# Optimization experiments

Hardware: AMD Instinct MI355X
Metric: run time of the kernel (lower is better)

## Reference

```python
import jax, jax.numpy as jnp
import numpy as np

B, S, T = 2048, 32, 32
D, H = 128, 256       # cle_dim, rnn_dim
VS, VT = 256, 256     # source/target char vocab
BOW = 1               # MorphoDataset.Factor.BOW


def setup_inputs() -> dict:
    key = jax.random.key(0)
    ks = jax.random.split(key, 16)
    n = lambda k, sh: (jax.random.normal(k, sh, jnp.float32) * 0.05)
    inp = {
        "src_emb": n(ks[0], (VS, D)),
        "tgt_emb": n(ks[1], (VT, D)),
        "enc_f_W": n(ks[2], (D, 3 * H)),
        "enc_f_U": n(ks[3], (H, 3 * H)),
        "enc_f_b": jnp.zeros((2, 3 * H), jnp.float32),
        "enc_b_W": n(ks[4], (D, 3 * H)),
        "enc_b_U": n(ks[5], (H, 3 * H)),
        "enc_b_b": jnp.zeros((2, 3 * H), jnp.float32),
        "dec_W": n(ks[6], (D + H, 3 * H)),
        "dec_U": n(ks[7], (H, 3 * H)),
        "dec_b": jnp.zeros((2, 3 * H), jnp.float32),
        "out_W": n(ks[8], (H, VT)),
        "out_b": jnp.zeros((VT,), jnp.float32),
        "att_src_W": n(ks[9], (H, H)),
        "att_src_b": jnp.zeros((H,), jnp.float32),
        "att_st_W": n(ks[10], (H, H)),
        "att_st_b": jnp.zeros((H,), jnp.float32),
        "att_v": n(ks[11], (H, 1)),
        "att_v_b": jnp.zeros((1,), jnp.float32),
        "source_ids": jax.random.randint(ks[12], (B, S), 0, VS, jnp.int32),
        "target_ids": jax.random.randint(ks[13], (B, T), 0, VT, jnp.int32),
    }
    return inp


def _gru_step(h, x, W, U, b):
    # Keras GRU, reset_after=True: separate input/recurrent biases b[0], b[1]
    gx = x @ W + b[0]
    gh = h @ U + b[1]
    xz, xr, xh = jnp.split(gx, 3, axis=-1)
    hz, hr, hh = jnp.split(gh, 3, axis=-1)
    z = jax.nn.sigmoid(xz + hz)
    r = jax.nn.sigmoid(xr + hr)
    c = jnp.tanh(xh + r * hh)
    return z * h + (1.0 - z) * c


def _gru_scan(x_tbd, W, U, b):
    # x_tbd: [S, B, D] -> outputs [S, B, H]
    h0 = jnp.zeros((x_tbd.shape[1], U.shape[0]), x_tbd.dtype)
    def step(h, x):
        h = _gru_step(h, x, W, U, b)
        return h, h
    _, ys = jax.lax.scan(step, h0, x_tbd)
    return ys


def reference(src_emb, tgt_emb, enc_f_W, enc_f_U, enc_f_b, enc_b_W, enc_b_U, enc_b_b,
              dec_W, dec_U, dec_b, out_W, out_b, att_src_W, att_src_b,
              att_st_W, att_st_b, att_v, att_v_b, source_ids, target_ids):
    # ---- Encoder: bidirectional GRU, merge_mode='sum' ----
    x = src_emb[source_ids]                      # [B, S, D]
    x_t = jnp.transpose(x, (1, 0, 2))            # [S, B, D]
    fwd = _gru_scan(x_t, enc_f_W, enc_f_U, enc_f_b)
    bwd = _gru_scan(x_t[::-1], enc_b_W, enc_b_U, enc_b_b)[::-1]
    source_states = jnp.transpose(fwd + bwd, (1, 0, 2))  # [B, S, H]

    # projected source states are constant across decoder steps -> precompute
    proj_src = source_states @ att_src_W + att_src_b     # [B, S, H]

    def attend(inp, h):
        p = h @ att_st_W + att_st_b                      # [B, H]
        e = jnp.tanh(proj_src + p[:, None, :]) @ att_v + att_v_b  # [B, S, 1]
        w = jax.nn.softmax(e, axis=1)                    # softmax over source positions
        ctx = jnp.sum(source_states * w, axis=1)         # [B, H]
        return jnp.concatenate([inp, ctx], axis=1)       # [B, D+H]

    # ---- Decoder (teacher forcing) ----
    h0 = source_states[:, 0]                             # [B, H]
    bow = jnp.broadcast_to(tgt_emb[BOW], (source_ids.shape[0], tgt_emb.shape[1]))
    inp0 = attend(bow, h0)

    def dstep(carry, tgt_t):
        h, inp = carry
        h = _gru_step(h, inp, dec_W, dec_U, dec_b)       # GRUCell step
        logits = h @ out_W + out_b                       # [B, VT]
        nxt = attend(tgt_emb[tgt_t], h)
        return (h, nxt), logits

    _, logits = jax.lax.scan(dstep, (h0, inp0), jnp.transpose(target_ids))
    return jnp.transpose(logits, (1, 0, 2))              # [B, T, VT]
```

## Files before the change

### kernel.cpp

```cpp
#include <hip/hip_runtime.h>
#include <math.h>

#define B_  2048
#define S_  32
#define T_  32
#define D_  128
#define H_  256
#define G3  768
#define VT_ 256
#define BOW_ 1

typedef __attribute__((ext_vector_type(8))) short short8;
typedef __attribute__((ext_vector_type(4))) float f32x4;
typedef __attribute__((ext_vector_type(8))) unsigned short us8;
typedef unsigned short u16;

__device__ inline u16 f2bf(float x) {
  union { float f; unsigned u; } v; v.f = x;
  unsigned r = v.u + 0x7FFFu + ((v.u >> 16) & 1u);
  return (u16)(r >> 16);
}
__device__ inline float bf2f(u16 b) {
  union { unsigned u; float f; } v; v.u = ((unsigned)b) << 16; return v.f;
}
__device__ inline int swz(int r) { return ((r ^ (r >> 3)) & 7) << 3; }
__device__ inline float sigm(float x) { return 1.f / (1.f + expf(-x)); }

struct TMat { const float* src; u16* dhi; u16* dlo; int R; int C; int tile0; };
struct TPack { TMat m[10]; };

__global__ __launch_bounds__(256)
void wsplit_t(TPack P) {
  int bx = blockIdx.x;
  TMat M = P.m[0];
  #pragma unroll
  for (int i = 1; i < 10; i++) if (bx >= P.m[i].tile0) M = P.m[i];
  int ti = bx - M.tile0;
  int tilesR = M.R >> 6;
  int rt = ti % tilesR, ct = ti / tilesR;
  int r0 = rt * 64, c0 = ct * 64;
  __shared__ float ts[64][65];
  int tid = threadIdx.x;
  int cx = tid & 63, ry = tid >> 6;
  #pragma unroll
  for (int i = 0; i < 16; i++) {
    int r = ry * 16 + i;
    ts[r][cx] = M.src[(size_t)(r0 + r) * M.C + c0 + cx];
  }
  __syncthreads();
  int rx = tid & 63, cy = tid >> 6;
  #pragma unroll
  for (int i = 0; i < 16; i++) {
    int cc = cy * 16 + i;
    float v = ts[rx][cc];
    u16 hi = f2bf(v);
    size_t o = (size_t)(c0 + cc) * M.R + r0 + rx;
    M.dhi[o] = hi;
    M.dlo[o] = f2bf(v - bf2f(hi));
  }
}

__global__ __launch_bounds__(256)
void esplit(const float* a, const float* b, u16* ah, u16* al, u16* bh, u16* bl, int n) {
  int i = blockIdx.x * 256 + threadIdx.x;
  if (i >= 2 * n) return;
  const float* s = (i < n) ? a : b;
  u16* dh = (i < n) ? ah : bh;
  u16* dl = (i < n) ? al : bl;
  int j = (i < n) ? i : i - n;
  float v = s[j];
  u16 hi = f2bf(v);
  dh[j] = hi; dl[j] = f2bf(v - bf2f(hi));
}

struct PLeg {
  const u16* Ahi; const u16* Alo; int lda;
  const u16* Bthi; const u16* Btlo; int ldb;
  const float* bias; void* C; int ldc; int cmode;
  int M, N, K;
};

__global__ __launch_bounds__(256)
void gemm_pl(PLeg l0, PLeg l1) {
  PLeg L = blockIdx.z ? l1 : l0;
  int n0 = blockIdx.x * 128; if (n0 >= L.N) return;
  int m0 = blockIdx.y * 128; if (m0 >= L.M) return;
  __shared__ u16 As[128 * 64];
  __shared__ u16 Bs[128 * 64];
  int tid = threadIdx.x;
  int lane = tid & 63, wv = tid >> 6;
  int wr = (wv >> 1) * 64, wc = (wv & 1) * 64;
  int fr = lane & 15, fk = (lane >> 4) * 8;
  f32x4 acc[4][4];
  #pragma unroll
  for (int m = 0; m < 4; m++)
    #pragma unroll
    for (int n = 0; n < 4; n++) acc[m][n] = (f32x4){0.f, 0.f, 0.f, 0.f};

  int s_row = tid >> 1, s_part = tid & 1;

  for (int k0 = 0; k0 < L.K; k0 += 32) {
    if (k0) __syncthreads();
    int swA = swz(s_row);
    {
      const u16* src = (s_part ? L.Alo : L.Ahi) + (size_t)(m0 + s_row) * L.lda + k0;
      #pragma unroll
      for (int q = 0; q < 4; q++)
        *(us8*)&As[(s_row * 64 + s_part * 32 + q * 8) ^ swA] = *(const us8*)(src + q * 8);
    }
    {
      const u16* src = (s_part ? L.Btlo : L.Bthi) + (size_t)(n0 + s_row) * L.ldb + k0;
      #pragma unroll
      for (int q = 0; q < 4; q++)
        *(us8*)&Bs[(s_row * 64 + s_part * 32 + q * 8) ^ swA] = *(const us8*)(src + q * 8);
    }
    __syncthreads();
    short8 bhi[4], blo[4];
    #pragma unroll
    for (int n = 0; n < 4; n++) {
      int cc = wc + n * 16 + fr; int sw = swz(cc);
      bhi[n] = *(const short8*)&Bs[(cc * 64 + fk) ^ sw];
      blo[n] = *(const short8*)&Bs[(cc * 64 + 32 + fk) ^ sw];
    }
    #pragma unroll
    for (int m = 0; m < 4; m++) {
      int r = wr + m * 16 + fr; int sw = swz(r);
      short8 ahi = *(const short8*)&As[(r * 64 + fk) ^ sw];
      short8 alo = *(const short8*)&As[(r * 64 + 32 + fk) ^ sw];
      #pragma unroll
      for (int n = 0; n < 4; n++) {
        acc[m][n] = __builtin_amdgcn_mfma_f32_16x16x32_bf16(ahi, bhi[n], acc[m][n], 0, 0, 0);
        acc[m][n] = __builtin_amdgcn_mfma_f32_16x16x32_bf16(ahi, blo[n], acc[m][n], 0, 0, 0);
        acc[m][n] = __builtin_amdgcn_mfma_f32_16x16x32_bf16(alo, bhi[n], acc[m][n], 0, 0, 0);
      }
    }
  }
  int rbase = (lane >> 4) * 4;
  #pragma unroll
  for (int m = 0; m < 4; m++)
    #pragma unroll
    for (int rr = 0; rr < 4; rr++) {
      int row = m0 + wr + m * 16 + rbase + rr;
      #pragma unroll
      for (int n = 0; n < 4; n++) {
        int col = n0 + wc + n * 16 + fr;
        float v = acc[m][n][rr];
        if (L.bias) v += L.bias[col];
        if (L.cmode == 0)      ((float*)L.C)[(size_t)row * L.ldc + col] = v;
        else if (L.cmode == 1) ((u16*)L.C)[(size_t)row * L.ldc + col] = f2bf(v);
        else {
          size_t o = (((size_t)(row & (B_ - 1))) * T_ + (row >> 11)) * VT_ + col;
          ((float*)L.C)[o] = v;
        }
      }
    }
}

struct GruDesc {
  const u16 *a0H, *a0L;
  const u16 *a1H, *a1L;
  const u16 *b0H, *b0L;
  const u16 *b1H, *b1L;
  const float *gxT;
  const float *bias0, *bias1;
  const float *hold;
  const u16 *holdH, *holdL;
  float *hnew;
  u16 *hh, *hl;
  u16 *ssH, *ssL;
  const int *ids;
  int ssmode;
  int sidx, rev;
};

template<int MODE>
__global__ __launch_bounds__(256)
void gru_step(GruDesc d0, GruDesc d1) {
  GruDesc D = blockIdx.z ? d1 : d0;
  constexpr int KT  = MODE ? 512 : 256;
  constexpr int KT8 = KT / 8;
  constexpr int MF  = MODE ? 1 : 2;
  constexpr int NST = KT / 32;
  __shared__ __align__(16) u16 As[2 * 32 * KT];

  int m0 = blockIdx.y * 32;
  int tid = threadIdx.x;
  int lane = tid & 63, wv = tid >> 6;
  int fr = lane & 15, kq = lane >> 4;
  int jn, rb0;
  if (MODE == 0) { jn = blockIdx.x * 64 + wv * 16 + fr; rb0 = 0; }
  else           { jn = blockIdx.x * 32 + (wv & 1) * 16 + fr; rb0 = (wv >> 1) * 16; }

  constexpr int PER_T = (2 * 32 * KT8) / 256;
  #pragma unroll
  for (int i = 0; i < PER_T; i++) {
    int s = tid + i * 256;
    int p = s / (32 * KT8);
    int rem = s - p * (32 * KT8);
    int row = rem / KT8;
    int kb = rem - row * KT8;
    int k = kb * 8;
    const u16* src;
    if (MODE == 0) {
      src = (p ? D.a0L : D.a0H) + (size_t)(m0 + row) * 256 + k;
    } else {
      src = (k < 256) ? (p ? D.a0L : D.a0H) + (size_t)(m0 + row) * 256 + k
                      : (p ? D.a1L : D.a1H) + (size_t)(m0 + row) * 256 + (k - 256);
    }
    *(us8*)&As[(s ^ (row & 7)) * 8] = *(const us8*)src;
  }
  __syncthreads();

  f32x4 acc[4][MF];
  #pragma unroll
  for (int a = 0; a < 4; a++)
    #pragma unroll
    for (int mf = 0; mf < MF; mf++) acc[a][mf] = (f32x4){0.f, 0.f, 0.f, 0.f};

  #pragma unroll
  for (int i = 0; i < NST; i++) {
    const u16 *BH, *BL; int bk, ai2;
    if (MODE == 0)    { BH = D.b0H; BL = D.b0L; bk = i * 32; ai2 = 2; }
    else if (i < 8)   { BH = D.b0H; BL = D.b0L; bk = i * 32; ai2 = 2; }
    else              { BH = D.b1H; BL = D.b1L; bk = (i - 8) * 32; ai2 = 3; }
    short8 ah[MF], al[MF];
    #pragma unroll
    for (int mf = 0; mf < MF; mf++) {
      int rp = rb0 + mf * 16 + fr;
      int kb = i * 4 + kq;
      ah[mf] = *(const short8*)&As[((rp * KT8 + kb) ^ (fr & 7)) * 8];
      al[mf] = *(const short8*)&As[((32 * KT8 + rp * KT8 + kb) ^ (fr & 7)) * 8];
    }
    #pragma unroll
    for (int st = 0; st < 3; st++) {
      size_t ro = (size_t)(st * 256 + jn) * 256 + bk + kq * 8;
      short8 bh = *(const short8*)(BH + ro);
      short8 bl = *(const short8*)(BL + ro);
      int ai = (st < 2) ? st : ai2;
      #pragma unroll
      for (int mf = 0; mf < MF; mf++) {
        acc[ai][mf] = __builtin_amdgcn_mfma_f32_16x16x32_bf16(ah[mf], bh, acc[ai][mf], 0, 0, 0);
        acc[ai][mf] = __builtin_amdgcn_mfma_f32_16x16x32_bf16(ah[mf], bl, acc[ai][mf], 0, 0, 0);
        acc[ai][mf] = __builtin_amdgcn_mfma_f32_16x16x32_bf16(al[mf], bh, acc[ai][mf], 0, 0, 0);
      }
    }
  }

  int rbase = kq * 4;
  int j = jn;
  float b0z = D.bias0[j],       b1z = D.bias1[j];
  float b0r = D.bias0[256 + j], b1r = D.bias1[256 + j];
  float b0c = D.bias0[512 + j], b1c = D.bias1[512 + j];
  #pragma unroll
  for (int mf = 0; mf < MF; mf++)
    #pragma unroll
    for (int rr = 0; rr < 4; rr++) {
      int b = m0 + rb0 + mf * 16 + rbase + rr;
      size_t o = (size_t)b * H_ + j;
      int id;
      if (MODE == 0) id = D.ids[b * S_ + (D.rev ? (S_ - 1 - D.sidx) : D.sidx)];
      else           id = (D.sidx == 0) ? BOW_ : D.ids[b * T_ + D.sidx - 1];
      const float* T = D.gxT + (size_t)id * G3;
      float z = sigm(acc[0][mf][rr] + T[j] + b0z + b1z);
      float r = sigm(acc[1][mf][rr] + T[256 + j] + b0r + b1r);
      float xc = T[512 + j] + b0c + (MODE ? acc[3][mf][rr] : 0.f);
      float c = tanhf(xc + r * (acc[2][mf][rr] + b1c));
      float hprev = D.hold ? D.hold[o] : (bf2f(D.holdH[o]) + bf2f(D.holdL[o]));
      float hn = z * hprev + (1.f - z) * c;
      D.hnew[o] = hn;
      u16 hi = f2bf(hn);
      D.hh[o] = hi; D.hl[o] = f2bf(hn - bf2f(hi));
      if (MODE == 0) {
        if (D.ssmode == 1) {
          D.ssH[o] = hi; D.ssL[o] = f2bf(hn - bf2f(hi));
        } else if (D.ssmode == 2) {
          float v = bf2f(D.ssH[o]) + bf2f(D.ssL[o]) + hn;
          u16 vh = f2bf(v);
          D.ssH[o] = vh; D.ssL[o] = f2bf(v - bf2f(vh));
        }
      }
    }
}

__global__ __launch_bounds__(256)
void attend_k(const u16* __restrict__ projbf, const u16* __restrict__ ssH,
              const float* __restrict__ p, const float* __restrict__ att_v,
              u16* __restrict__ ctxh, u16* __restrict__ ctxl) {
  int b = blockIdx.x;
  int tid = threadIdx.x;
  int lane = tid & 63;
  int wv = tid >> 6;
  __shared__ float e_s[S_];
  __shared__ float w_s[S_];
  float pq[4], vq[4];
  #pragma unroll
  for (int q = 0; q < 4; q++) {
    pq[q] = p[(size_t)b * H_ + q * 64 + lane];
    vq[q] = att_v[q * 64 + lane];
  }
  float pv[8][4];
  #pragma unroll
  for (int i = 0; i < 8; i++) {
    const u16* pr = projbf + ((size_t)(wv * 8 + i) * B_ + b) * H_;
    #pragma unroll
    for (int q = 0; q < 4; q++) pv[i][q] = bf2f(pr[q * 64 + lane]);
  }
  u16 sv[S_];
  #pragma unroll
  for (int s = 0; s < S_; s++) sv[s] = ssH[((size_t)s * B_ + b) * H_ + tid];

  #pragma unroll
  for (int i = 0; i < 8; i++) {
    float part = 0.f;
    #pragma unroll
    for (int q = 0; q < 4; q++)
      part += tanhf(pv[i][q] + pq[q]) * vq[q];
    #pragma unroll
    for (int off = 32; off; off >>= 1)
      part += __shfl_xor(part, off);
    if (lane == 0) e_s[wv * 8 + i] = part;
  }
  __syncthreads();
  float m = -1e30f;
  #pragma unroll
  for (int s = 0; s < S_; s++) m = fmaxf(m, e_s[s]);
  float den = 0.f;
  #pragma unroll
  for (int s = 0; s < S_; s++) den += expf(e_s[s] - m);
  if (tid < S_) w_s[tid] = expf(e_s[tid] - m) / den;
  __syncthreads();
  float acc = 0.f;
  #pragma unroll
  for (int s = 0; s < S_; s++)
    acc = fmaf(w_s[s], bf2f(sv[s]), acc);
  u16 hi = f2bf(acc);
  size_t o = (size_t)b * H_ + tid;
  ctxh[o] = hi; ctxl[o] = f2bf(acc - bf2f(hi));
}

extern "C" void kernel_launch(void* const* d_in, const int* in_sizes, int n_in,
                              void* d_out, int out_size, void* d_ws, size_t ws_size,
                              hipStream_t stream) {
  const float* src_emb   = (const float*)d_in[0];
  const float* tgt_emb   = (const float*)d_in[1];
  const float* enc_f_W   = (const float*)d_in[2];
  const float* enc_f_U   = (const float*)d_in[3];
  const float* enc_f_b   = (const float*)d_in[4];
  const float* enc_b_W   = (const float*)d_in[5];
  const float* enc_b_U   = (const float*)d_in[6];
  const float* enc_b_b   = (const float*)d_in[7];
  const float* dec_W     = (const float*)d_in[8];
  const float* dec_U     = (const float*)d_in[9];
  const float* dec_b     = (const float*)d_in[10];
  const float* out_W     = (const float*)d_in[11];
  const float* out_b     = (const float*)d_in[12];
  const float* att_src_W = (const float*)d_in[13];
  const float* att_src_b = (const float*)d_in[14];
  const float* att_st_W  = (const float*)d_in[15];
  const float* att_st_b  = (const float*)d_in[16];
  const float* att_v     = (const float*)d_in[17];
  const int* source_ids  = (const int*)d_in[19];
  const int* target_ids  = (const int*)d_in[20];
  float* out = (float*)d_out;

  char* base = (char*)d_ws;
  size_t off = 0;
  auto allocB = [&](size_t bytes) { void* p = base + off; off = (off + bytes + 255) & ~255UL; return p; };
  const size_t BH = (size_t)B_ * H_;

  u16* ssH    = (u16*)allocB((size_t)S_ * BH * 2);
  u16* ssL    = (u16*)allocB((size_t)S_ * BH * 2);
  u16* projbf = (u16*)allocB((size_t)S_ * BH * 2);
  float* pbuf = (float*)allocB(BH * 4);
  u16* ctxh = (u16*)allocB(BH * 2);
  u16* ctxl = (u16*)allocB(BH * 2);

  float* encF0 = (float*)allocB(2 * BH * 4);
  u16*  encPl0 = (u16*)allocB(4 * BH * 2);
  float* encF1 = (float*)allocB(2 * BH * 4);
  u16*  encPl1 = (u16*)allocB(4 * BH * 2);
  float* encF[2][2]  = { { encF0, encF0 + BH }, { encF1, encF1 + BH } };
  u16*  encH[2][2]   = { { encPl0, encPl0 + 2 * BH }, { encPl1, encPl1 + 2 * BH } };
  u16*  encL[2][2]   = { { encPl0 + BH, encPl0 + 3 * BH }, { encPl1 + BH, encPl1 + 3 * BH } };

  float* hDecF[2] = { (float*)allocB(BH * 4), (float*)allocB(BH * 4) };
  u16* hAllH = (u16*)allocB((size_t)T_ * BH * 2);
  u16* hAllL = (u16*)allocB((size_t)T_ * BH * 2);

  auto planes2 = [&](size_t n, u16*& h, u16*& l) { h = (u16*)allocB(n * 2); l = (u16*)allocB(n * 2); };
  u16 *UtFh,*UtFl,*UtBh,*UtBl,*WtFh,*WtFl,*WtBh,*WtBl;
  u16 *dUth,*dUtl,*dWcth,*dWctl,*dWxth,*dWxtl;
  u16 *oWth,*oWtl,*aStth,*aSttl,*aSrth,*aSrtl;
  u16 *sEh,*sEl,*tEh,*tEl;
  planes2((size_t)G3*H_, UtFh, UtFl);   planes2((size_t)G3*H_, UtBh, UtBl);
  planes2((size_t)G3*D_, WtFh, WtFl);   planes2((size_t)G3*D_, WtBh, WtBl);
  planes2((size_t)G3*H_, dUth, dUtl);   planes2((size_t)G3*H_, dWcth, dWctl);
  planes2((size_t)G3*D_, dWxth, dWxtl);
  planes2((size_t)H_*VT_, oWth, oWtl);
  planes2((size_t)H_*H_, aSrth, aSrtl);
  planes2((size_t)H_*H_, aStth, aSttl);
  planes2((size_t)VT_*D_, sEh, sEl);    planes2((size_t)VT_*D_, tEh, tEl);
  float* Tf = (float*)allocB((size_t)VT_ * G3 * 4);
  float* Tb = (float*)allocB((size_t)VT_ * G3 * 4);
  float* Td = (float*)allocB((size_t)VT_ * G3 * 4);

  TPack P;
  P.m[0] = { enc_f_U,          UtFh, UtFl, 256, 768, 0   };
  P.m[1] = { enc_b_U,          UtBh, UtBl, 256, 768, 48  };
  P.m[2] = { dec_U,            dUth, dUtl, 256, 768, 96  };
  P.m[3] = { dec_W + 128 * G3, dWcth, dWctl, 256, 768, 144 };
  P.m[4] = { enc_f_W,          WtFh, WtFl, 128, 768, 192 };
  P.m[5] = { enc_b_W,          WtBh, WtBl, 128, 768, 216 };
  P.m[6] = { dec_W,            dWxth, dWxtl, 128, 768, 240 };
  P.m[7] = { out_W,            oWth, oWtl, 256, 256, 264 };
  P.m[8] = { att_src_W,        aSrth, aSrtl, 256, 256, 280 };
  P.m[9] = { att_st_W,         aStth, aSttl, 256, 256, 296 };
  wsplit_t<<<312, 256, 0, stream>>>(P);
  esplit<<<(2 * VT_ * D_ + 255) / 256, 256, 0, stream>>>(src_emb, tgt_emb, sEh, sEl, tEh, tEl, VT_ * D_);

  {
    PLeg tf = { sEh, sEl, D_, WtFh, WtFl, D_, nullptr, Tf, G3, 0, VT_, G3, D_ };
    PLeg tb = { sEh, sEl, D_, WtBh, WtBl, D_, nullptr, Tb, G3, 0, VT_, G3, D_ };
    gemm_pl<<<dim3(6, 2, 2), 256, 0, stream>>>(tf, tb);
    PLeg td = { tEh, tEl, D_, dWxth, dWxtl, D_, nullptr, Td, G3, 0, VT_, G3, D_ };
    gemm_pl<<<dim3(6, 2, 1), 256, 0, stream>>>(td, td);
  }

  hipMemsetAsync(encF0, 0, 2 * BH * 4, stream);
  hipMemsetAsync(encPl0, 0, 4 * BH * 2, stream);

  for (int s = 0; s < S_; s++) {
    int p = s & 1;
    GruDesc dd[2];
    for (int d = 0; d < 2; d++) {
      GruDesc& D = dd[d];
      D.a0H = encH[p][d]; D.a0L = encL[p][d];
      D.a1H = nullptr; D.a1L = nullptr;
      D.b0H = d ? UtBh : UtFh; D.b0L = d ? UtBl : UtFl;
      D.b1H = nullptr; D.b1L = nullptr;
      D.gxT = d ? Tb : Tf;
      D.bias0 = d ? enc_b_b : enc_f_b;
      D.bias1 = (d ? enc_b_b : enc_f_b) + G3;
      D.hold = encF[p][d]; D.holdH = nullptr; D.holdL = nullptr;
      D.hnew = encF[p ^ 1][d];
      D.hh = encH[p ^ 1][d]; D.hl = encL[p ^ 1][d];
      int pos = d ? (S_ - 1 - s) : s;
      D.ssH = ssH + (size_t)pos * BH; D.ssL = ssL + (size_t)pos * BH;
      D.ids = source_ids;
      D.ssmode = (s < S_ / 2) ? 1 : 2;
      D.sidx = s; D.rev = d;
    }
    gru_step<0><<<dim3(4, 64, 2), 256, 0, stream>>>(dd[0], dd[1]);
  }

  {
    PLeg proj = { ssH, ssL, H_, aSrth, aSrtl, H_, att_src_b, projbf, H_, 1, S_ * B_, H_, H_ };
    PLeg p0   = { ssH, ssL, H_, aStth, aSttl, H_, att_st_b,  pbuf,   H_, 0, B_,      H_, H_ };
    gemm_pl<<<dim3(2, 512, 2), 256, 0, stream>>>(proj, p0);
  }
  attend_k<<<B_, 256, 0, stream>>>(projbf, ssH, pbuf, att_v, ctxh, ctxl);

  for (int t = 0; t < T_; t++) {
    int p = t & 1;
    GruDesc D = {};
    D.a0H = t ? hAllH + (size_t)(t - 1) * BH : ssH;
    D.a0L = t ? hAllL + (size_t)(t - 1) * BH : ssL;
    D.a1H = ctxh; D.a1L = ctxl;
    D.b0H = dUth;  D.b0L = dUtl;
    D.b1H = dWcth; D.b1L = dWctl;
    D.gxT = Td;
    D.bias0 = dec_b; D.bias1 = dec_b + G3;
    if (t == 0) { D.hold = nullptr; D.holdH = ssH; D.holdL = ssL; }
    else        { D.hold = hDecF[p]; D.holdH = nullptr; D.holdL = nullptr; }
    D.hnew = hDecF[p ^ 1];
    D.hh = hAllH + (size_t)t * BH; D.hl = hAllL + (size_t)t * BH;
    D.ssH = nullptr; D.ssL = nullptr;
    D.ids = target_ids;
    D.ssmode = 0; D.sidx = t; D.rev = 0;
    gru_step<1><<<dim3(8, 64, 1), 256, 0, stream>>>(D, D);

    if (t < T_ - 1) {
      PLeg LP = { hAllH + (size_t)t * BH, hAllL + (size_t)t * BH, H_,
                  aStth, aSttl, H_, att_st_b, pbuf, H_, 0, B_, H_, H_ };
      gemm_pl<<<dim3(2, 16, 1), 256, 0, stream>>>(LP, LP);
      attend_k<<<B_, 256, 0, stream>>>(projbf, ssH, pbuf, att_v, ctxh, ctxl);
    }
  }

  {
    PLeg LO = { hAllH, hAllL, H_, oWth, oWtl, H_, out_b, out, 0, 2, T_ * B_, VT_, H_ };
    gemm_pl<<<dim3(2, 512, 1), 256, 0, stream>>>(LO, LO);
  }
}
```

Before: 3.604 ms.

## Replace per-step GRU launches with persistent encoder and decoder kernels

```diff
diff --git a/kernel.cpp b/kernel.cpp
--- a/kernel.cpp
+++ b/kernel.cpp
@@ -15,6 +15,8 @@
 typedef __attribute__((ext_vector_type(8))) unsigned short us8;
 typedef unsigned short u16;
 
+#define MFMA16 __builtin_amdgcn_mfma_f32_16x16x32_bf16
+
 __device__ inline u16 f2bf(float x) {
   union { float f; unsigned u; } v; v.f = x;
   unsigned r = v.u + 0x7FFFu + ((v.u >> 16) & 1u);
@@ -24,6 +26,9 @@
   union { unsigned u; float f; } v; v.u = ((unsigned)b) << 16; return v.f;
 }
 __device__ inline int swz(int r) { return ((r ^ (r >> 3)) & 7) << 3; }
+__device__ inline int psl(int row, int j) {
+  return row * 256 + ((((j >> 3) ^ (row & 7)) << 3) | (j & 7));
+}
 __device__ inline float sigm(float x) { return 1.f / (1.f + expf(-x)); }
 
 struct TMat { const float* src; u16* dhi; u16* dlo; int R; int C; int tile0; };
@@ -129,9 +134,9 @@
       short8 alo = *(const short8*)&As[(r * 64 + 32 + fk) ^ sw];
       #pragma unroll
       for (int n = 0; n < 4; n++) {
-        acc[m][n] = __builtin_amdgcn_mfma_f32_16x16x32_bf16(ahi, bhi[n], acc[m][n], 0, 0, 0);
-        acc[m][n] = __builtin_amdgcn_mfma_f32_16x16x32_bf16(ahi, blo[n], acc[m][n], 0, 0, 0);
-        acc[m][n] = __builtin_amdgcn_mfma_f32_16x16x32_bf16(alo, bhi[n], acc[m][n], 0, 0, 0);
+        acc[m][n] = MFMA16(ahi, bhi[n], acc[m][n], 0, 0, 0);
+        acc[m][n] = MFMA16(ahi, blo[n], acc[m][n], 0, 0, 0);
+        acc[m][n] = MFMA16(alo, bhi[n], acc[m][n], 0, 0, 0);
       }
     }
   }
@@ -156,186 +161,332 @@
     }
 }
 
-struct GruDesc {
-  const u16 *a0H, *a0L;
-  const u16 *a1H, *a1L;
-  const u16 *b0H, *b0L;
-  const u16 *b1H, *b1L;
-  const float *gxT;
+struct EncMP {
+  const u16 *UH0, *UL0, *UH1, *UL1;
+  const float *gxT0, *gxT1;
   const float *bias0, *bias1;
-  const float *hold;
-  const u16 *holdH, *holdL;
-  float *hnew;
-  u16 *hh, *hl;
   u16 *ssH, *ssL;
   const int *ids;
-  int ssmode;
-  int sidx, rev;
 };
 
-template<int MODE>
-__global__ __launch_bounds__(256)
-void gru_step(GruDesc d0, GruDesc d1) {
-  GruDesc D = blockIdx.z ? d1 : d0;
-  constexpr int KT  = MODE ? 512 : 256;
-  constexpr int KT8 = KT / 8;
-  constexpr int MF  = MODE ? 1 : 2;
-  constexpr int NST = KT / 32;
-  __shared__ __align__(16) u16 As[2 * 32 * KT];
-
-  int m0 = blockIdx.y * 32;
-  int tid = threadIdx.x;
-  int lane = tid & 63, wv = tid >> 6;
-  int fr = lane & 15, kq = lane >> 4;
-  int jn, rb0;
-  if (MODE == 0) { jn = blockIdx.x * 64 + wv * 16 + fr; rb0 = 0; }
-  else           { jn = blockIdx.x * 32 + (wv & 1) * 16 + fr; rb0 = (wv >> 1) * 16; }
-
-  constexpr int PER_T = (2 * 32 * KT8) / 256;
-  #pragma unroll
-  for (int i = 0; i < PER_T; i++) {
-    int s = tid + i * 256;
-    int p = s / (32 * KT8);
-    int rem = s - p * (32 * KT8);
-    int row = rem / KT8;
-    int kb = rem - row * KT8;
-    int k = kb * 8;
-    const u16* src;
-    if (MODE == 0) {
-      src = (p ? D.a0L : D.a0H) + (size_t)(m0 + row) * 256 + k;
-    } else {
-      src = (k < 256) ? (p ? D.a0L : D.a0H) + (size_t)(m0 + row) * 256 + k
-                      : (p ? D.a1L : D.a1H) + (size_t)(m0 + row) * 256 + (k - 256);
-    }
-    *(us8*)&As[(s ^ (row & 7)) * 8] = *(const us8*)src;
-  }
+__global__ __launch_bounds__(256, 1)
+void enc_mono(EncMP P) {
+  __shared__ __align__(16) u16 hPl[2][2][4096];
+  __shared__ float hF[2][2048];
+  __shared__ int ids_l[256];
+  const int tid = threadIdx.x;
+  const int lane = tid & 63, wv = tid >> 6;
+  const int fr = lane & 15, kq = lane >> 4;
+  const int jb = wv * 64;
+  const int r0 = blockIdx.x * 8;
+
+  {
+    us8 z8 = {0,0,0,0,0,0,0,0};
+    us8* pb = (us8*)&hPl[0][0][0];
+    #pragma unroll
+    for (int i = 0; i < 8; i++) pb[i * 256 + tid] = z8;
+    f32x4 zf = {0.f,0.f,0.f,0.f};
+    f32x4* fb = (f32x4*)&hF[0][0];
+    #pragma unroll
+    for (int i = 0; i < 4; i++) fb[i * 256 + tid] = zf;
+  }
+  ids_l[tid] = P.ids[(r0 + (tid >> 5)) * S_ + (tid & 31)];
   __syncthreads();
 
-  f32x4 acc[4][MF];
-  #pragma unroll
-  for (int a = 0; a < 4; a++)
-    #pragma unroll
-    for (int mf = 0; mf < MF; mf++) acc[a][mf] = (f32x4){0.f, 0.f, 0.f, 0.f};
-
-  #pragma unroll
-  for (int i = 0; i < NST; i++) {
-    const u16 *BH, *BL; int bk, ai2;
-    if (MODE == 0)    { BH = D.b0H; BL = D.b0L; bk = i * 32; ai2 = 2; }
-    else if (i < 8)   { BH = D.b0H; BL = D.b0L; bk = i * 32; ai2 = 2; }
-    else              { BH = D.b1H; BL = D.b1L; bk = (i - 8) * 32; ai2 = 3; }
-    short8 ah[MF], al[MF];
-    #pragma unroll
-    for (int mf = 0; mf < MF; mf++) {
-      int rp = rb0 + mf * 16 + fr;
-      int kb = i * 4 + kq;
-      ah[mf] = *(const short8*)&As[((rp * KT8 + kb) ^ (fr & 7)) * 8];
-      al[mf] = *(const short8*)&As[((32 * KT8 + rp * KT8 + kb) ^ (fr & 7)) * 8];
-    }
-    #pragma unroll
-    for (int st = 0; st < 3; st++) {
-      size_t ro = (size_t)(st * 256 + jn) * 256 + bk + kq * 8;
-      short8 bh = *(const short8*)(BH + ro);
-      short8 bl = *(const short8*)(BL + ro);
-      int ai = (st < 2) ? st : ai2;
-      #pragma unroll
-      for (int mf = 0; mf < MF; mf++) {
-        acc[ai][mf] = __builtin_amdgcn_mfma_f32_16x16x32_bf16(ah[mf], bh, acc[ai][mf], 0, 0, 0);
-        acc[ai][mf] = __builtin_amdgcn_mfma_f32_16x16x32_bf16(ah[mf], bl, acc[ai][mf], 0, 0, 0);
-        acc[ai][mf] = __builtin_amdgcn_mfma_f32_16x16x32_bf16(al[mf], bh, acc[ai][mf], 0, 0, 0);
-      }
-    }
-  }
-
-  int rbase = kq * 4;
-  int j = jn;
-  float b0z = D.bias0[j],       b1z = D.bias1[j];
-  float b0r = D.bias0[256 + j], b1r = D.bias1[256 + j];
-  float b0c = D.bias0[512 + j], b1c = D.bias1[512 + j];
-  #pragma unroll
-  for (int mf = 0; mf < MF; mf++)
-    #pragma unroll
-    for (int rr = 0; rr < 4; rr++) {
-      int b = m0 + rb0 + mf * 16 + rbase + rr;
-      size_t o = (size_t)b * H_ + j;
-      int id;
-      if (MODE == 0) id = D.ids[b * S_ + (D.rev ? (S_ - 1 - D.sidx) : D.sidx)];
-      else           id = (D.sidx == 0) ? BOW_ : D.ids[b * T_ + D.sidx - 1];
-      const float* T = D.gxT + (size_t)id * G3;
-      float z = sigm(acc[0][mf][rr] + T[j] + b0z + b1z);
-      float r = sigm(acc[1][mf][rr] + T[256 + j] + b0r + b1r);
-      float xc = T[512 + j] + b0c + (MODE ? acc[3][mf][rr] : 0.f);
-      float c = tanhf(xc + r * (acc[2][mf][rr] + b1c));
-      float hprev = D.hold ? D.hold[o] : (bf2f(D.holdH[o]) + bf2f(D.holdL[o]));
-      float hn = z * hprev + (1.f - z) * c;
-      D.hnew[o] = hn;
-      u16 hi = f2bf(hn);
-      D.hh[o] = hi; D.hl[o] = f2bf(hn - bf2f(hi));
-      if (MODE == 0) {
-        if (D.ssmode == 1) {
-          D.ssH[o] = hi; D.ssL[o] = f2bf(hn - bf2f(hi));
-        } else if (D.ssmode == 2) {
-          float v = bf2f(D.ssH[o]) + bf2f(D.ssL[o]) + hn;
-          u16 vh = f2bf(v);
-          D.ssH[o] = vh; D.ssL[o] = f2bf(v - bf2f(vh));
+  float bz[2][4], br[2][4], bxc[2][4], bhc[2][4];
+  #pragma unroll
+  for (int d = 0; d < 2; d++) {
+    const float* b0 = d ? P.bias1 : P.bias0;
+    const float* b1 = b0 + G3;
+    #pragma unroll
+    for (int nt = 0; nt < 4; nt++) {
+      int j = jb + nt * 16 + fr;
+      bz[d][nt]  = b0[j] + b1[j];
+      br[d][nt]  = b0[256 + j] + b1[256 + j];
+      bxc[d][nt] = b0[512 + j];
+      bhc[d][nt] = b1[512 + j];
+    }
+  }
+
+  for (int s = 0; s < S_; s++) {
+    #pragma unroll 1
+    for (int d = 0; d < 2; d++) {
+      const u16* UH = d ? P.UH1 : P.UH0;
+      const u16* UL = d ? P.UL1 : P.UL0;
+      const float* gxT = d ? P.gxT1 : P.gxT0;
+      u16* hp0 = hPl[d][0];
+      u16* hp1 = hPl[d][1];
+      f32x4 acc[3][4];
+      #pragma unroll
+      for (int a = 0; a < 3; a++)
+        #pragma unroll
+        for (int nt = 0; nt < 4; nt++) acc[a][nt] = (f32x4){0.f,0.f,0.f,0.f};
+
+      #pragma unroll
+      for (int i = 0; i < 8; i++) {
+        int slot = (((i * 4 + kq) ^ (fr & 7)) << 3);
+        short8 ah = *(const short8*)&hp0[fr * 256 + slot];
+        short8 al = *(const short8*)&hp1[fr * 256 + slot];
+        #pragma unroll
+        for (int st = 0; st < 3; st++)
+          #pragma unroll
+          for (int nt = 0; nt < 4; nt++) {
+            size_t ro = (size_t)(st * 256 + jb + nt * 16 + fr) * 256 + i * 32 + kq * 8;
+            short8 bh = *(const short8*)(UH + ro);
+            short8 bl = *(const short8*)(UL + ro);
+            acc[st][nt] = MFMA16(ah, bh, acc[st][nt], 0, 0, 0);
+            acc[st][nt] = MFMA16(ah, bl, acc[st][nt], 0, 0, 0);
+            acc[st][nt] = MFMA16(al, bh, acc[st][nt], 0, 0, 0);
+          }
+      }
+      __syncthreads();
+      if (kq < 2) {
+        #pragma unroll
+        for (int rr = 0; rr < 4; rr++) {
+          int row = kq * 4 + rr;
+          int gb = r0 + row;
+          int id = ids_l[row * 32 + (d ? (31 - s) : s)];
+          const float* T = gxT + (size_t)id * G3;
+          int pos = d ? (31 - s) : s;
+          #pragma unroll
+          for (int nt = 0; nt < 4; nt++) {
+            int j = jb + nt * 16 + fr;
+            float z = sigm(acc[0][nt][rr] + T[j] + bz[d][nt]);
+            float r = sigm(acc[1][nt][rr] + T[256 + j] + br[d][nt]);
+            float c = tanhf(T[512 + j] + bxc[d][nt] + r * (acc[2][nt][rr] + bhc[d][nt]));
+            float hp = hF[d][row * 256 + j];
+            float hn = z * hp + (1.f - z) * c;
+            hF[d][row * 256 + j] = hn;
+            u16 hi = f2bf(hn);
+            u16 lo = f2bf(hn - bf2f(hi));
+            int ps = psl(row, j);
+            hp0[ps] = hi; hp1[ps] = lo;
+            size_t o = ((size_t)pos * B_ + gb) * 256 + j;
+            if (s < 16) {
+              P.ssH[o] = hi; P.ssL[o] = lo;
+            } else {
+              float v = bf2f(P.ssH[o]) + bf2f(P.ssL[o]) + hn;
+              u16 vh = f2bf(v);
+              P.ssH[o] = vh; P.ssL[o] = f2bf(v - bf2f(vh));
+            }
+          }
         }
       }
-    }
-}
-
-__global__ __launch_bounds__(256)
-void attend_k(const u16* __restrict__ projbf, const u16* __restrict__ ssH,
-              const float* __restrict__ p, const float* __restrict__ att_v,
-              u16* __restrict__ ctxh, u16* __restrict__ ctxl) {
-  int b = blockIdx.x;
-  int tid = threadIdx.x;
-  int lane = tid & 63;
-  int wv = tid >> 6;
-  __shared__ float e_s[S_];
-  __shared__ float w_s[S_];
-  float pq[4], vq[4];
-  #pragma unroll
-  for (int q = 0; q < 4; q++) {
-    pq[q] = p[(size_t)b * H_ + q * 64 + lane];
-    vq[q] = att_v[q * 64 + lane];
-  }
-  float pv[8][4];
-  #pragma unroll
-  for (int i = 0; i < 8; i++) {
-    const u16* pr = projbf + ((size_t)(wv * 8 + i) * B_ + b) * H_;
-    #pragma unroll
-    for (int q = 0; q < 4; q++) pv[i][q] = bf2f(pr[q * 64 + lane]);
-  }
-  u16 sv[S_];
-  #pragma unroll
-  for (int s = 0; s < S_; s++) sv[s] = ssH[((size_t)s * B_ + b) * H_ + tid];
-
-  #pragma unroll
-  for (int i = 0; i < 8; i++) {
-    float part = 0.f;
-    #pragma unroll
-    for (int q = 0; q < 4; q++)
-      part += tanhf(pv[i][q] + pq[q]) * vq[q];
-    #pragma unroll
-    for (int off = 32; off; off >>= 1)
-      part += __shfl_xor(part, off);
-    if (lane == 0) e_s[wv * 8 + i] = part;
-  }
+      __syncthreads();
+    }
+  }
+}
+
+struct DecMP {
+  const u16 *UH, *UL, *CH, *CL;
+  const float *gxT;
+  const float *bias;
+  const u16 *sWH, *sWL;
+  const float *stb;
+  const u16 *ssH, *ssL;
+  const u16 *projbf;
+  const float *attv;
+  u16 *hAH, *hAL;
+  const int *ids;
+};
+
+__global__ __launch_bounds__(256, 1)
+void dec_mono(DecMP P) {
+  __shared__ __align__(16) u16 hPl[2][4096];
+  __shared__ __align__(16) u16 cPl[2][4096];
+  __shared__ float hF[2048];
+  __shared__ float pS[2048];
+  __shared__ int ids_l[256];
+  const int tid = threadIdx.x;
+  const int lane = tid & 63, wv = tid >> 6;
+  const int fr = lane & 15, kq = lane >> 4;
+  const int jb = wv * 64;
+  const int r0 = blockIdx.x * 8;
+
+  {
+    us8 z8 = {0,0,0,0,0,0,0,0};
+    us8* pb = (us8*)&hPl[0][0];
+    #pragma unroll
+    for (int i = 0; i < 4; i++) pb[i * 256 + tid] = z8;
+    us8* cb = (us8*)&cPl[0][0];
+    #pragma unroll
+    for (int i = 0; i < 4; i++) cb[i * 256 + tid] = z8;
+  }
+  ids_l[tid] = P.ids[(r0 + (tid >> 5)) * T_ + (tid & 31)];
   __syncthreads();
-  float m = -1e30f;
-  #pragma unroll
-  for (int s = 0; s < S_; s++) m = fmaxf(m, e_s[s]);
-  float den = 0.f;
-  #pragma unroll
-  for (int s = 0; s < S_; s++) den += expf(e_s[s] - m);
-  if (tid < S_) w_s[tid] = expf(e_s[tid] - m) / den;
+  {
+    int row = tid >> 5;
+    int k = (tid & 31) * 8;
+    size_t go = ((size_t)(r0 + row)) * 256 + k;
+    us8 hv = *(const us8*)(P.ssH + go);
+    us8 lv = *(const us8*)(P.ssL + go);
+    int sl = row * 256 + ((((k >> 3) ^ (row & 7))) << 3);
+    *(us8*)&hPl[0][sl] = hv;
+    *(us8*)&hPl[1][sl] = lv;
+    #pragma unroll
+    for (int e = 0; e < 8; e++) hF[row * 256 + k + e] = bf2f(hv[e]) + bf2f(lv[e]);
+  }
+
+  float bz[4], br_[4], bxc[4], bhc[4], stbv[4];
+  #pragma unroll
+  for (int nt = 0; nt < 4; nt++) {
+    int j = jb + nt * 16 + fr;
+    bz[nt]  = P.bias[j] + P.bias[G3 + j];
+    br_[nt] = P.bias[256 + j] + P.bias[G3 + 256 + j];
+    bxc[nt] = P.bias[512 + j];
+    bhc[nt] = P.bias[G3 + 512 + j];
+    stbv[nt] = P.stb[j];
+  }
+  float vq[4];
+  #pragma unroll
+  for (int q = 0; q < 4; q++) vq[q] = P.attv[q * 64 + lane];
   __syncthreads();
-  float acc = 0.f;
-  #pragma unroll
-  for (int s = 0; s < S_; s++)
-    acc = fmaf(w_s[s], bf2f(sv[s]), acc);
-  u16 hi = f2bf(acc);
-  size_t o = (size_t)b * H_ + tid;
-  ctxh[o] = hi; ctxl[o] = f2bf(acc - bf2f(hi));
+
+  auto lp_attend = [&]() {
+    f32x4 pa[4];
+    #pragma unroll
+    for (int nt = 0; nt < 4; nt++) pa[nt] = (f32x4){0.f,0.f,0.f,0.f};
+    #pragma unroll
+    for (int i = 0; i < 8; i++) {
+      int slot = (((i * 4 + kq) ^ (fr & 7)) << 3);
+      short8 ah = *(const short8*)&hPl[0][fr * 256 + slot];
+      short8 al = *(const short8*)&hPl[1][fr * 256 + slot];
+      #pragma unroll
+      for (int nt = 0; nt < 4; nt++) {
+        size_t ro = (size_t)(jb + nt * 16 + fr) * 256 + i * 32 + kq * 8;
+        short8 bh = *(const short8*)(P.sWH + ro);
+        short8 bl = *(const short8*)(P.sWL + ro);
+        pa[nt] = MFMA16(ah, bh, pa[nt], 0, 0, 0);
+        pa[nt] = MFMA16(ah, bl, pa[nt], 0, 0, 0);
+        pa[nt] = MFMA16(al, bh, pa[nt], 0, 0, 0);
+      }
+    }
+    if (kq < 2) {
+      #pragma unroll
+      for (int rr = 0; rr < 4; rr++) {
+        int row = kq * 4 + rr;
+        #pragma unroll
+        for (int nt = 0; nt < 4; nt++) {
+          int j = jb + nt * 16 + fr;
+          pS[row * 256 + j] = pa[nt][rr] + stbv[nt];
+        }
+      }
+    }
+    __syncthreads();
+    #pragma unroll 1
+    for (int u = 0; u < 2; u++) {
+      int row = wv * 2 + u;
+      int gb = r0 + row;
+      float pq[4];
+      #pragma unroll
+      for (int q = 0; q < 4; q++) pq[q] = pS[row * 256 + q * 64 + lane];
+      float sc[S_];
+      #pragma unroll
+      for (int s2 = 0; s2 < S_; s2++) {
+        const u16* pr = P.projbf + ((size_t)s2 * B_ + gb) * 256;
+        float part = 0.f;
+        #pragma unroll
+        for (int q = 0; q < 4; q++)
+          part += tanhf(bf2f(pr[q * 64 + lane]) + pq[q]) * vq[q];
+        #pragma unroll
+        for (int off = 32; off; off >>= 1)
+          part += __shfl_xor(part, off);
+        sc[s2] = part;
+      }
+      float m = -1e30f;
+      #pragma unroll
+      for (int s2 = 0; s2 < S_; s2++) m = fmaxf(m, sc[s2]);
+      float den = 0.f;
+      #pragma unroll
+      for (int s2 = 0; s2 < S_; s2++) { sc[s2] = expf(sc[s2] - m); den += sc[s2]; }
+      float inv = 1.f / den;
+      float cacc[4] = {0.f, 0.f, 0.f, 0.f};
+      #pragma unroll
+      for (int s2 = 0; s2 < S_; s2++) {
+        float w = sc[s2] * inv;
+        const u16* sp = P.ssH + ((size_t)s2 * B_ + gb) * 256;
+        #pragma unroll
+        for (int q = 0; q < 4; q++)
+          cacc[q] = fmaf(w, bf2f(sp[q * 64 + lane]), cacc[q]);
+      }
+      #pragma unroll
+      for (int q = 0; q < 4; q++) {
+        int j = q * 64 + lane;
+        u16 hi = f2bf(cacc[q]);
+        int ps = psl(row, j);
+        cPl[0][ps] = hi;
+        cPl[1][ps] = f2bf(cacc[q] - bf2f(hi));
+      }
+    }
+  };
+
+  lp_attend();
+  __syncthreads();
+
+  for (int t = 0; t < T_; t++) {
+    f32x4 acc[4][4];
+    #pragma unroll
+    for (int a = 0; a < 4; a++)
+      #pragma unroll
+      for (int nt = 0; nt < 4; nt++) acc[a][nt] = (f32x4){0.f,0.f,0.f,0.f};
+
+    #pragma unroll
+    for (int i = 0; i < 16; i++) {
+      const u16* BH = (i < 8) ? P.UH : P.CH;
+      const u16* BL = (i < 8) ? P.UL : P.CL;
+      const u16* a0p = (i < 8) ? hPl[0] : cPl[0];
+      const u16* a1p = (i < 8) ? hPl[1] : cPl[1];
+      int ii = i & 7;
+      int slot = (((ii * 4 + kq) ^ (fr & 7)) << 3);
+      short8 ah = *(const short8*)&a0p[fr * 256 + slot];
+      short8 al = *(const short8*)&a1p[fr * 256 + slot];
+      int ci = (i < 8) ? 2 : 3;
+      #pragma unroll
+      for (int st = 0; st < 3; st++) {
+        int ai = (st < 2) ? st : ci;
+        #pragma unroll
+        for (int nt = 0; nt < 4; nt++) {
+          size_t ro = (size_t)(st * 256 + jb + nt * 16 + fr) * 256 + ii * 32 + kq * 8;
+          short8 bh = *(const short8*)(BH + ro);
+          short8 bl = *(const short8*)(BL + ro);
+          acc[ai][nt] = MFMA16(ah, bh, acc[ai][nt], 0, 0, 0);
+          acc[ai][nt] = MFMA16(ah, bl, acc[ai][nt], 0, 0, 0);
+          acc[ai][nt] = MFMA16(al, bh, acc[ai][nt], 0, 0, 0);
+        }
+      }
+    }
+    __syncthreads();
+    if (kq < 2) {
+      #pragma unroll
+      for (int rr = 0; rr < 4; rr++) {
+        int row = kq * 4 + rr;
+        int gb = r0 + row;
+        int id = (t == 0) ? BOW_ : ids_l[row * 32 + t - 1];
+        const float* T = P.gxT + (size_t)id * G3;
+        #pragma unroll
+        for (int nt = 0; nt < 4; nt++) {
+          int j = jb + nt * 16 + fr;
+          float z = sigm(acc[0][nt][rr] + T[j] + bz[nt]);
+          float r = sigm(acc[1][nt][rr] + T[256 + j] + br_[nt]);
+          float c = tanhf(T[512 + j] + bxc[nt] + acc[3][nt][rr] + r * (acc[2][nt][rr] + bhc[nt]));
+          float hp = hF[row * 256 + j];
+          float hn = z * hp + (1.f - z) * c;
+          hF[row * 256 + j] = hn;
+          u16 hi = f2bf(hn);
+          u16 lo = f2bf(hn - bf2f(hi));
+          int ps = psl(row, j);
+          hPl[0][ps] = hi; hPl[1][ps] = lo;
+          size_t o = ((size_t)t * B_ + gb) * 256 + j;
+          P.hAH[o] = hi; P.hAL[o] = lo;
+        }
+      }
+    }
+    __syncthreads();
+    if (t < T_ - 1) {
+      lp_attend();
+      __syncthreads();
+    }
+  }
 }
 
 extern "C" void kernel_launch(void* const* d_in, const int* in_sizes, int n_in,
@@ -371,21 +522,8 @@
   u16* ssH    = (u16*)allocB((size_t)S_ * BH * 2);
   u16* ssL    = (u16*)allocB((size_t)S_ * BH * 2);
   u16* projbf = (u16*)allocB((size_t)S_ * BH * 2);
-  float* pbuf = (float*)allocB(BH * 4);
-  u16* ctxh = (u16*)allocB(BH * 2);
-  u16* ctxl = (u16*)allocB(BH * 2);
-
-  float* encF0 = (float*)allocB(2 * BH * 4);
-  u16*  encPl0 = (u16*)allocB(4 * BH * 2);
-  float* encF1 = (float*)allocB(2 * BH * 4);
-  u16*  encPl1 = (u16*)allocB(4 * BH * 2);
-  float* encF[2][2]  = { { encF0, encF0 + BH }, { encF1, encF1 + BH } };
-  u16*  encH[2][2]   = { { encPl0, encPl0 + 2 * BH }, { encPl1, encPl1 + 2 * BH } };
-  u16*  encL[2][2]   = { { encPl0 + BH, encPl0 + 3 * BH }, { encPl1 + BH, encPl1 + 3 * BH } };
-
-  float* hDecF[2] = { (float*)allocB(BH * 4), (float*)allocB(BH * 4) };
-  u16* hAllH = (u16*)allocB((size_t)T_ * BH * 2);
-  u16* hAllL = (u16*)allocB((size_t)T_ * BH * 2);
+  u16* hAllH  = (u16*)allocB((size_t)T_ * BH * 2);
+  u16* hAllL  = (u16*)allocB((size_t)T_ * BH * 2);
 
   auto planes2 = [&](size_t n, u16*& h, u16*& l) { h = (u16*)allocB(n * 2); l = (u16*)allocB(n * 2); };
   u16 *UtFh,*UtFl,*UtBh,*UtBl,*WtFh,*WtFl,*WtBh,*WtBl;
@@ -426,65 +564,34 @@
     gemm_pl<<<dim3(6, 2, 1), 256, 0, stream>>>(td, td);
   }
 
-  hipMemsetAsync(encF0, 0, 2 * BH * 4, stream);
-  hipMemsetAsync(encPl0, 0, 4 * BH * 2, stream);
-
-  for (int s = 0; s < S_; s++) {
-    int p = s & 1;
-    GruDesc dd[2];
-    for (int d = 0; d < 2; d++) {
-      GruDesc& D = dd[d];
-      D.a0H = encH[p][d]; D.a0L = encL[p][d];
-      D.a1H = nullptr; D.a1L = nullptr;
-      D.b0H = d ? UtBh : UtFh; D.b0L = d ? UtBl : UtFl;
-      D.b1H = nullptr; D.b1L = nullptr;
-      D.gxT = d ? Tb : Tf;
-      D.bias0 = d ? enc_b_b : enc_f_b;
-      D.bias1 = (d ? enc_b_b : enc_f_b) + G3;
-      D.hold = encF[p][d]; D.holdH = nullptr; D.holdL = nullptr;
-      D.hnew = encF[p ^ 1][d];
-      D.hh = encH[p ^ 1][d]; D.hl = encL[p ^ 1][d];
-      int pos = d ? (S_ - 1 - s) : s;
-      D.ssH = ssH + (size_t)pos * BH; D.ssL = ssL + (size_t)pos * BH;
-      D.ids = source_ids;
-      D.ssmode = (s < S_ / 2) ? 1 : 2;
-      D.sidx = s; D.rev = d;
-    }
-    gru_step<0><<<dim3(4, 64, 2), 256, 0, stream>>>(dd[0], dd[1]);
+  {
+    EncMP Pe;
+    Pe.UH0 = UtFh; Pe.UL0 = UtFl; Pe.UH1 = UtBh; Pe.UL1 = UtBl;
+    Pe.gxT0 = Tf; Pe.gxT1 = Tb;
+    Pe.bias0 = enc_f_b; Pe.bias1 = enc_b_b;
+    Pe.ssH = ssH; Pe.ssL = ssL;
+    Pe.ids = source_ids;
+    enc_mono<<<256, 256, 0, stream>>>(Pe);
   }
 
   {
     PLeg proj = { ssH, ssL, H_, aSrth, aSrtl, H_, att_src_b, projbf, H_, 1, S_ * B_, H_, H_ };
-    PLeg p0   = { ssH, ssL, H_, aStth, aSttl, H_, att_st_b,  pbuf,   H_, 0, B_,      H_, H_ };
-    gemm_pl<<<dim3(2, 512, 2), 256, 0, stream>>>(proj, p0);
-  }
-  attend_k<<<B_, 256, 0, stream>>>(projbf, ssH, pbuf, att_v, ctxh, ctxl);
-
-  for (int t = 0; t < T_; t++) {
-    int p = t & 1;
-    GruDesc D = {};
-    D.a0H = t ? hAllH + (size_t)(t - 1) * BH : ssH;
-    D.a0L = t ? hAllL + (size_t)(t - 1) * BH : ssL;
-    D.a1H = ctxh; D.a1L = ctxl;
-    D.b0H = dUth;  D.b0L = dUtl;
-    D.b1H = dWcth; D.b1L = dWctl;
-    D.gxT = Td;
-    D.bias0 = dec_b; D.bias1 = dec_b + G3;
-    if (t == 0) { D.hold = nullptr; D.holdH = ssH; D.holdL = ssL; }
-    else        { D.hold = hDecF[p]; D.holdH = nullptr; D.holdL = nullptr; }
-    D.hnew = hDecF[p ^ 1];
-    D.hh = hAllH + (size_t)t * BH; D.hl = hAllL + (size_t)t * BH;
-    D.ssH = nullptr; D.ssL = nullptr;
-    D.ids = target_ids;
-    D.ssmode = 0; D.sidx = t; D.rev = 0;
-    gru_step<1><<<dim3(8, 64, 1), 256, 0, stream>>>(D, D);
-
-    if (t < T_ - 1) {
-      PLeg LP = { hAllH + (size_t)t * BH, hAllL + (size_t)t * BH, H_,
-                  aStth, aSttl, H_, att_st_b, pbuf, H_, 0, B_, H_, H_ };
-      gemm_pl<<<dim3(2, 16, 1), 256, 0, stream>>>(LP, LP);
-      attend_k<<<B_, 256, 0, stream>>>(projbf, ssH, pbuf, att_v, ctxh, ctxl);
-    }
+    gemm_pl<<<dim3(2, 512, 1), 256, 0, stream>>>(proj, proj);
+  }
+
+  {
+    DecMP Pd;
+    Pd.UH = dUth; Pd.UL = dUtl; Pd.CH = dWcth; Pd.CL = dWctl;
+    Pd.gxT = Td;
+    Pd.bias = dec_b;
+    Pd.sWH = aStth; Pd.sWL = aSttl;
+    Pd.stb = att_st_b;
+    Pd.ssH = ssH; Pd.ssL = ssL;
+    Pd.projbf = projbf;
+    Pd.attv = att_v;
+    Pd.hAH = hAllH; Pd.hAL = hAllL;
+    Pd.ids = target_ids;
+    dec_mono<<<256, 256, 0, stream>>>(Pd);
   }
 
   {
```

Measured after the change: 12.23 ms. 3.4x slower.
